# Kernel optimization log

Hardware: AMD Instinct MI355X
Metric: run time of the kernel (lower is better)

## Reference

```python
import jax, jax.numpy as jnp
import numpy as np

LN_EPS = 1e-5

def _ln(x):
    # haiku LayerNorm([-1], create_scale=False, create_offset=False)
    mu = x.mean(axis=-1, keepdims=True)
    var = x.var(axis=-1, keepdims=True)
    return (x - mu) * jax.lax.rsqrt(var + LN_EPS)

def setup_inputs() -> dict:
    key = jax.random.key(0)
    ks = jax.random.split(key, 10)
    N, L, P = 512, 256, 64
    inp = {
        "local": jax.random.normal(ks[0], (N, L), jnp.float32),
        "pair": jax.random.normal(ks[1], (N, N, P), jnp.float32),
        "mask": jax.random.randint(ks[2], (N,), 0, 2, jnp.int32),
        "W_pair_gate": jax.random.normal(ks[3], (P, 2 * P), jnp.float32) / np.sqrt(P),
        "W_pair_value": jax.random.normal(ks[4], (P, 2 * P), jnp.float32) / np.sqrt(P),
        "W_left_gate": jax.random.normal(ks[5], (L, 2 * P), jnp.float32) / np.sqrt(L),
        "W_left_value": jax.random.normal(ks[6], (L, 2 * P), jnp.float32) / np.sqrt(L),
        "W_right_gate": jax.random.normal(ks[7], (L, 2 * P), jnp.float32) / np.sqrt(L),
        "W_right_value": jax.random.normal(ks[8], (L, 2 * P), jnp.float32) / np.sqrt(L),
        "W_out": jax.random.normal(ks[9], (3 * P, P), jnp.float32) / np.sqrt(3 * P),
    }
    return inp

def reference(local, pair, mask, W_pair_gate, W_pair_value, W_left_gate,
              W_left_value, W_right_gate, W_right_value, W_out):
    maskb = mask.astype(bool)
    pair_mask = maskb[:, None] & maskb[None, :]                  # (N, N)
    l = _ln(local)                                               # (N, L)
    p = _ln(pair)                                                # (N, N, P)
    pair_gate = p @ W_pair_gate                                  # (N, N, 2P)
    pair_value = p @ W_pair_value                                # (N, N, 2P)
    # left: broadcast local over axis 0/1, gelu-gate, mask, reduce over j
    left_gate = jax.nn.gelu((l @ W_left_gate)[:, None] + pair_gate)
    left_value = (l @ W_left_value)[None, :] + pair_value
    left = jnp.where(pair_mask[..., None], left_gate * left_value, 0).sum(axis=1)  # (N, 2P)
    right_gate = jax.nn.gelu((l @ W_right_gate)[None, :] + pair_gate)
    right_value = (l @ W_right_value)[:, None] + pair_value
    right = jnp.where(pair_mask[..., None], right_gate * right_value, 0).sum(axis=0)  # (N, 2P)
    paired_pseudo_local = _ln(left[:, None] + right[None, :])    # (N, N, 2P)
    pair_hidden = jnp.concatenate((p, paired_pseudo_local), axis=-1)  # (N, N, 3P)
    return pair_hidden @ W_out                                   # (N, N, P)
```

## Files before the change

### kernel.cpp

```cpp
#include <hip/hip_runtime.h>
#include <math.h>

#define LN_EPS 1e-5f


typedef __bf16 bf16x8 __attribute__((ext_vector_type(8)));
typedef float f32x16 __attribute__((ext_vector_type(16)));

__device__ __forceinline__ float gelu_f(float x) {
    float x2 = x * x;
    float e = __builtin_amdgcn_exp2f(x * fmaf(0.10294423f, x2, 2.3022079f));
    float r = __builtin_amdgcn_rcpf(e + 1.0f);
    return fmaf(-x, r, x);
}

__global__ __launch_bounds__(256) void kA(
    const float* __restrict__ loc,
    const float* __restrict__ Wlg, const float* __restrict__ Wlv,
    const float* __restrict__ Wrg, const float* __restrict__ Wrv,
    float* __restrict__ proj, const int* __restrict__ mask,
    int* __restrict__ act, float* __restrict__ left, float* __restrict__ right) {
    const int t = threadIdx.x;
    if (blockIdx.x == 64) {
        if (blockIdx.y == 1) {
            float4 z = {0.f, 0.f, 0.f, 0.f};
            for (int idx = t; idx < 16384; idx += 256) ((float4*)left)[idx] = z;
        } else if (blockIdx.y == 2) {
            float4 z = {0.f, 0.f, 0.f, 0.f};
            for (int idx = t; idx < 16384; idx += 256) ((float4*)right)[idx] = z;
        } else if (blockIdx.y == 0) {
            __shared__ int cnt_sh[8];
            const int lane = t & 63, wv = t >> 6;
            int msave[2];
            unsigned long long bsave[2];
#pragma unroll
            for (int ch = 0; ch < 2; ++ch) {
                int m = (mask[ch * 256 + t] != 0);
                unsigned long long b = __ballot(m);
                if (lane == 0) cnt_sh[ch * 4 + wv] = __popcll(b);
                msave[ch] = m;
                bsave[ch] = b;
            }
            __syncthreads();
#pragma unroll
            for (int ch = 0; ch < 2; ++ch) {
                int base = 0;
                for (int u = 0; u < ch * 4 + wv; ++u) base += cnt_sh[u];
                int pos = base + __popcll(bsave[ch] & ((1ull << lane) - 1ull));
                if (msave[ch]) act[1 + pos] = ch * 256 + t;
            }
            if (t == 0) {
                int ctot = 0;
                for (int u = 0; u < 8; ++u) ctot += cnt_sh[u];
                act[0] = ctot;
            }
        }
        return;
    }
    __shared__ float ln_sh[8][260];
    __shared__ float red_sh[128][9];
    const int i0 = blockIdx.x * 8;
    const int mat = blockIdx.y;
    const float* __restrict__ W = (mat == 0) ? Wlg : (mat == 1) ? Wlv
                                 : (mat == 2) ? Wrg : Wrv;
    {
        int row = t >> 5, l32 = t & 31;
        const float4* src = (const float4*)(loc + (i0 + row) * 256);
        float4 v0 = src[l32 * 2];
        float4 v1 = src[l32 * 2 + 1];
        float s = (v0.x + v0.y) + (v0.z + v0.w) + (v1.x + v1.y) + (v1.z + v1.w);
        float ss = v0.x * v0.x + v0.y * v0.y + v0.z * v0.z + v0.w * v0.w +
                   v1.x * v1.x + v1.y * v1.y + v1.z * v1.z + v1.w * v1.w;
#pragma unroll
        for (int off = 1; off < 32; off <<= 1) {
            s += __shfl_xor(s, off);
            ss += __shfl_xor(ss, off);
        }
        float mu = s * (1.f / 256.f);
        float rs = rsqrtf(ss * (1.f / 256.f) - mu * mu + LN_EPS);
        float4 o0, o1;
        o0.x = (v0.x - mu) * rs; o0.y = (v0.y - mu) * rs;
        o0.z = (v0.z - mu) * rs; o0.w = (v0.w - mu) * rs;
        o1.x = (v1.x - mu) * rs; o1.y = (v1.y - mu) * rs;
        o1.z = (v1.z - mu) * rs; o1.w = (v1.w - mu) * rs;
        *(float4*)&ln_sh[row][l32 * 8] = o0;
        *(float4*)&ln_sh[row][l32 * 8 + 4] = o1;
    }
    __syncthreads();

    const int n = t & 127;
    const int kh = t >> 7;
    float acc[8] = {0.f, 0.f, 0.f, 0.f, 0.f, 0.f, 0.f, 0.f};
#pragma unroll 2
    for (int c = 0; c < 32; ++c) {
        const int kc = kh * 128 + c * 4;
        float w0 = W[(kc + 0) * 128 + n];
        float w1 = W[(kc + 1) * 128 + n];
        float w2 = W[(kc + 2) * 128 + n];
        float w3 = W[(kc + 3) * 128 + n];
#pragma unroll
        for (int r = 0; r < 8; ++r) {
            float4 l4 = *(const float4*)&ln_sh[r][kc];
            acc[r] += l4.x * w0 + l4.y * w1 + l4.z * w2 + l4.w * w3;
        }
    }
    if (kh == 1) {
#pragma unroll
        for (int r = 0; r < 8; ++r) red_sh[n][r] = acc[r];
    }
    __syncthreads();
    if (kh == 0) {
#pragma unroll
        for (int r = 0; r < 8; ++r)
            proj[mat * 65536 + (i0 + r) * 128 + n] = acc[r] + red_sh[n][r];
    }
}

#define KB_TI 4
__global__ __launch_bounds__(256) void kB(
    const float* __restrict__ pair, const int* __restrict__ act,
    const float* __restrict__ Wg, const float* __restrict__ Wv,
    const float* __restrict__ lg, const float* __restrict__ lv,
    const float* __restrict__ rg, const float* __restrict__ rv,
    float* __restrict__ left, float* __restrict__ right) {
    __shared__ __bf16 A_sh[2][32][72];
    __shared__ int ji_sh[32];
    __shared__ int ii_sh[KB_TI];

    const int cnt = act[0];
    const int j0 = blockIdx.x * 32;
    const int ibase = blockIdx.y * KB_TI;
    if (j0 >= cnt || ibase >= cnt) return;
    const int nact = min(KB_TI, cnt - ibase);

    const int t = threadIdx.x;
    const int lane = t & 63;
    const int w = t >> 6;
    const int c = lane & 31;
    const int half = lane >> 5;
    const int n = w * 32 + c;

    if (t < 32) ji_sh[t] = act[1 + min(j0 + t, cnt - 1)];
    if (t >= 64 && t < 64 + KB_TI) ii_sh[t - 64] = act[1 + min(ibase + (t - 64), cnt - 1)];
    __syncthreads();

    bf16x8 bg[4], bv[4];
#pragma unroll
    for (int kt = 0; kt < 4; ++kt) {
        bf16x8 vg, vv;
#pragma unroll
        for (int e = 0; e < 8; ++e) {
            int kr = kt * 16 + half * 8 + e;
            vg[e] = (__bf16)Wg[kr * 128 + n];
            vv[e] = (__bf16)Wv[kr * 128 + n];
        }
        bg[kt] = vg; bv[kt] = vv;
    }

    float lvr[16], rgr[16];
    unsigned jmask = 0;
#pragma unroll
    for (int r = 0; r < 16; ++r) {
        int m = 4 * half + (r & 3) + 8 * (r >> 2);
        int j = ji_sh[m];
        lvr[r] = lv[j * 128 + n];
        rgr[r] = rg[j * 128 + n];
        if (j0 + m < cnt) jmask |= (1u << r);
    }

    const int srow = t >> 3;
    const int kseg = (t & 7) * 8;
    float4 p0, p1;
    float plg, prv;
    {
        int iF = ii_sh[0];
        const float* src = pair + ((size_t)iF * 512 + ji_sh[srow]) * 64 + kseg;
        p0 = *(const float4*)src;
        p1 = *(const float4*)(src + 4);
        plg = lg[iF * 128 + n];
        prv = rv[iF * 128 + n];
    }

    auto lnwrite = [&](int buf) {
        float s = (p0.x + p0.y) + (p0.z + p0.w) + (p1.x + p1.y) + (p1.z + p1.w);
        float ss = p0.x * p0.x + p0.y * p0.y + p0.z * p0.z + p0.w * p0.w +
                   p1.x * p1.x + p1.y * p1.y + p1.z * p1.z + p1.w * p1.w;
        s += __shfl_xor(s, 1); ss += __shfl_xor(ss, 1);
        s += __shfl_xor(s, 2); ss += __shfl_xor(ss, 2);
        s += __shfl_xor(s, 4); ss += __shfl_xor(ss, 4);
        float mu = s * (1.f / 64.f);
        float rs = rsqrtf(ss * (1.f / 64.f) - mu * mu + LN_EPS);
        bf16x8 o;
        o[0] = (__bf16)((p0.x - mu) * rs); o[1] = (__bf16)((p0.y - mu) * rs);
        o[2] = (__bf16)((p0.z - mu) * rs); o[3] = (__bf16)((p0.w - mu) * rs);
        o[4] = (__bf16)((p1.x - mu) * rs); o[5] = (__bf16)((p1.y - mu) * rs);
        o[6] = (__bf16)((p1.z - mu) * rs); o[7] = (__bf16)((p1.w - mu) * rs);
        *(bf16x8*)&A_sh[buf][srow][kseg] = o;
    };
    lnwrite(0);
    __syncthreads();

    float racc[16];
#pragma unroll
    for (int r = 0; r < 16; ++r) racc[r] = 0.f;

    for (int ii = 0; ii < nact; ++ii) {
        const int i = ii_sh[ii];
        const float lgi = plg;
        const float rvi = prv;
        if (ii + 1 < nact) {
            int iF = ii_sh[ii + 1];
            const float* src = pair + ((size_t)iF * 512 + ji_sh[srow]) * 64 + kseg;
            p0 = *(const float4*)src;
            p1 = *(const float4*)(src + 4);
            plg = lg[iF * 128 + n];
            prv = rv[iF * 128 + n];
        }

        f32x16 ag = {}; f32x16 av = {};
#pragma unroll
        for (int kt = 0; kt < 4; ++kt) {
            bf16x8 af = *(const bf16x8*)&A_sh[ii & 1][c][kt * 16 + half * 8];
            ag = __builtin_amdgcn_mfma_f32_32x32x16_bf16(af, bg[kt], ag, 0, 0, 0);
            av = __builtin_amdgcn_mfma_f32_32x32x16_bf16(af, bv[kt], av, 0, 0, 0);
        }

        float lsum = 0.f;
#pragma unroll
        for (int r = 0; r < 16; ++r) {
            float pg = ag[r], pv = av[r];
            float lres = gelu_f(lgi + pg) * (lvr[r] + pv);
            float rres = gelu_f(rgr[r] + pg) * (rvi + pv);
            lsum += ((jmask >> r) & 1) ? lres : 0.f;
            racc[r] += rres;
        }
        float tot = lsum + __shfl_xor(lsum, 32);
        if (lane < 32) atomicAdd(&left[i * 128 + n], tot);

        if (ii + 1 < nact) lnwrite((ii + 1) & 1);
        __syncthreads();
    }

#pragma unroll
    for (int r = 0; r < 16; ++r) {
        if ((jmask >> r) & 1) {
            int m = 4 * half + (r & 3) + 8 * (r >> 2);
            atomicAdd(&right[ji_sh[m] * 128 + n], racc[r]);
        }
    }
}

__global__ __launch_bounds__(256) void kD(
    const float* __restrict__ left, const float* __restrict__ right,
    const float* __restrict__ W_out,
    float* __restrict__ Aw, float* __restrict__ Bw,
    float* __restrict__ rsArr, float* __restrict__ rmArr,
    float* __restrict__ cs) {
    const int bx = blockIdx.x;
    const int t = threadIdx.x;
    if (bx < 256) {
        __shared__ float l_sh[32][68];
        __shared__ float r_sh[32][68];
        const int tx = t & 15, ty = t >> 4;
        const int i0 = (bx & 15) * 32, j0 = (bx >> 4) * 32;
        float acc00 = 0.f, acc01 = 0.f, acc10 = 0.f, acc11 = 0.f;
        float sL0 = 0.f, ssL0 = 0.f, sL1 = 0.f, ssL1 = 0.f;
        float sR0 = 0.f, ssR0 = 0.f, sR1 = 0.f, ssR1 = 0.f;
        for (int kc = 0; kc < 128; kc += 64) {
            __syncthreads();
#pragma unroll
            for (int u = 0; u < 2; ++u) {
                int fi = t + u * 256;
                int row = fi >> 4, kq = (fi & 15) * 4;
                float4 lv4 = *(const float4*)(left + (i0 + row) * 128 + kc + kq);
                float4 rv4 = *(const float4*)(right + (j0 + row) * 128 + kc + kq);
                *(float4*)&l_sh[row][kq] = lv4;
                *(float4*)&r_sh[row][kq] = rv4;
            }
            __syncthreads();
#pragma unroll 8
            for (int k = 0; k < 64; ++k) {
                float l0 = l_sh[ty * 2 + 0][k], l1 = l_sh[ty * 2 + 1][k];
                float r0 = r_sh[tx * 2 + 0][k], r1 = r_sh[tx * 2 + 1][k];
                acc00 += l0 * r0; acc01 += l0 * r1;
                acc10 += l1 * r0; acc11 += l1 * r1;
                sL0 += l0; ssL0 += l0 * l0;
                sL1 += l1; ssL1 += l1 * l1;
                sR0 += r0; ssR0 += r0 * r0;
                sR1 += r1; ssR1 += r1 * r1;
            }
        }
        {
            float sLa[2] = {sL0, sL1}, ssLa[2] = {ssL0, ssL1};
            float sRb[2] = {sR0, sR1}, ssRb[2] = {ssR0, ssR1};
            float accv[2][2] = {{acc00, acc01}, {acc10, acc11}};
#pragma unroll
            for (int a = 0; a < 2; ++a) {
#pragma unroll
                for (int b = 0; b < 2; ++b) {
                    float mu = (sLa[a] + sRb[b]) * (1.f / 128.f);
                    float var = fmaf(-mu, mu,
                                     (ssLa[a] + 2.f * accv[a][b] + ssRb[b]) * (1.f / 128.f));
                    float rs = rsqrtf(var + LN_EPS);
                    size_t idx = (size_t)(i0 + ty * 2 + a) * 512 + (j0 + tx * 2 + b);
                    rsArr[idx] = rs;
                    rmArr[idx] = rs * mu;
                }
            }
        }
    } else {
        const int id = bx - 256;
        const int which = id >> 8;
        const int sub = t >> 7;
        const int tt = t & 127;
        const int r = (id & 255) * 2 + sub;
        const float* src = which ? right : left;
        __shared__ float row_sh[2][128];
        row_sh[sub][tt] = src[r * 128 + tt];
        __syncthreads();
        if (tt < 64) {
            float a = 0.f;
            const float* W2 = W_out + 64 * 64;
#pragma unroll 8
            for (int m = 0; m < 128; ++m) a += row_sh[sub][m] * W2[m * 64 + tt];
            (which ? Bw : Aw)[r * 64 + tt] = a;
        }
        if (id == 0 && t < 64) {
            float c0 = 0.f, c1 = 0.f;
            for (int k = 0; k < 64; ++k) c0 += W_out[k * 64 + t];
            for (int m = 0; m < 128; ++m) c1 += W_out[(64 + m) * 64 + t];
            cs[t] = c0;
            cs[64 + t] = c1;
        }
    }
}

__global__ __launch_bounds__(256) void kC(
    const float* __restrict__ pair, const float* __restrict__ Wout,
    const float* __restrict__ Aw, const float* __restrict__ Bw,
    const float* __restrict__ rsArr, const float* __restrict__ rmArr,
    const float* __restrict__ cs, float* __restrict__ out) {
    const int t = threadIdx.x;
    const int lane = t & 63;
    const int w = t >> 6;
    const int c = lane & 31;
    const int half = lane >> 5;
    const int i0 = blockIdx.x * 4;
    const int j0 = blockIdx.y * 64;
    const int mt = w & 1;
    const int nt = w >> 1;
    const int n = nt * 32 + c;
    const int jrow = j0 + mt * 32 + c;

    const float* __restrict__ abase = pair + ((size_t)i0 * 512 + jrow) * 64 + half * 8;

    float4 va[8], vb[8];
#pragma unroll
    for (int kt = 0; kt < 4; ++kt) {
        va[2 * kt] = *(const float4*)(abase + kt * 16);
        va[2 * kt + 1] = *(const float4*)(abase + kt * 16 + 4);
    }

    bf16x8 bo[4];
#pragma unroll
    for (int kt = 0; kt < 4; ++kt) {
        bf16x8 bb;
#pragma unroll
        for (int e = 0; e < 8; ++e)
            bb[e] = (__bf16)Wout[(kt * 16 + half * 8 + e) * 64 + n];
        bo[kt] = bb;
    }
    float Bv[16];
#pragma unroll
    for (int r = 0; r < 16; ++r) {
        int jp = j0 + mt * 32 + 4 * half + (r & 3) + 8 * (r >> 2);
        Bv[r] = Bw[jp * 64 + n];
    }
    const float cs1n = cs[64 + n];

    auto body = [&](float4 (&cur)[8], float4 (&nxt)[8], int ii) {
        if (ii < 3) {
            const float* src = abase + (size_t)(ii + 1) * 512 * 64;
#pragma unroll
            for (int kt = 0; kt < 4; ++kt) {
                nxt[2 * kt] = *(const float4*)(src + kt * 16);
                nxt[2 * kt + 1] = *(const float4*)(src + kt * 16 + 4);
            }
        }
        const int i = i0 + ii;
        const float A_in = Aw[i * 64 + n];

        float s = 0.f, ss = 0.f;
#pragma unroll
        for (int u = 0; u < 8; ++u) {
            s += (cur[u].x + cur[u].y) + (cur[u].z + cur[u].w);
            ss += cur[u].x * cur[u].x + cur[u].y * cur[u].y +
                  cur[u].z * cur[u].z + cur[u].w * cur[u].w;
        }
        s += __shfl_xor(s, 32);
        ss += __shfl_xor(ss, 32);
        float mu = s * (1.f / 64.f);
        float rs = rsqrtf(ss * (1.f / 64.f) - mu * mu + LN_EPS);

        f32x16 acc = {};
#pragma unroll
        for (int kt = 0; kt < 4; ++kt) {
            bf16x8 af;
#pragma unroll
            for (int u = 0; u < 2; ++u) {
                float4 vv = cur[2 * kt + u];
                af[u * 4 + 0] = (__bf16)((vv.x - mu) * rs);
                af[u * 4 + 1] = (__bf16)((vv.y - mu) * rs);
                af[u * 4 + 2] = (__bf16)((vv.z - mu) * rs);
                af[u * 4 + 3] = (__bf16)((vv.w - mu) * rs);
            }
            acc = __builtin_amdgcn_mfma_f32_32x32x16_bf16(af, bo[kt], acc, 0, 0, 0);
        }

#pragma unroll
        for (int r = 0; r < 16; ++r) {
            int jp = j0 + mt * 32 + 4 * half + (r & 3) + 8 * (r >> 2);
            size_t idx = (size_t)i * 512 + jp;
            float rsv = rsArr[idx];
            float rmv = rmArr[idx];
            out[idx * 64 + n] =
                fmaf(rsv, A_in + Bv[r], fmaf(-rmv, cs1n, acc[r]));
        }
    };
    body(va, vb, 0);
    body(vb, va, 1);
    body(va, vb, 2);
    body(vb, va, 3);
}

extern "C" void kernel_launch(void* const* d_in, const int* in_sizes, int n_in,
                              void* d_out, int out_size, void* d_ws, size_t ws_size,
                              hipStream_t stream) {
    const float* loc  = (const float*)d_in[0];
    const float* pair = (const float*)d_in[1];
    const int*   mask = (const int*)d_in[2];
    const float* Wpg  = (const float*)d_in[3];
    const float* Wpv  = (const float*)d_in[4];
    const float* Wlg  = (const float*)d_in[5];
    const float* Wlv  = (const float*)d_in[6];
    const float* Wrg  = (const float*)d_in[7];
    const float* Wrv  = (const float*)d_in[8];
    const float* Wout = (const float*)d_in[9];
    float* out = (float*)d_out;
    float* ws = (float*)d_ws;

    float* proj  = ws;
    float* left  = ws + 262144;
    float* right = ws + 327680;
    float* Aw    = ws + 393216;
    float* Bw    = ws + 425984;
    float* rsA   = ws + 458752;
    float* rmA   = ws;
    float* cs    = ws + 722944;
    int*   act   = (int*)(ws + 723072);

    kA<<<dim3(65, 4), 256, 0, stream>>>(loc, Wlg, Wlv, Wrg, Wrv, proj,
                                        mask, act, left, right);
    kB<<<dim3(16, 128), 256, 0, stream>>>(pair, act, Wpg, Wpv,
                                          proj, proj + 65536, proj + 131072,
                                          proj + 196608, left, right);
    kD<<<768, 256, 0, stream>>>(left, right, Wout, Aw, Bw, rsA, rmA, cs);
    kC<<<dim3(128, 8), 256, 0, stream>>>(pair, Wout, Aw, Bw, rsA, rmA, cs, out);
}
```

Before: 190.9 us.

## Privatize right-side atomic accumulation into eight partial buffers reduced in kD

The right-reduction atomics in kB now go to one of eight private copies of the right buffer, chosen by blockIdx.y, instead of a single shared buffer. kD sums the eight partials when it loads right. The aim is to cut atomic contention on the same addresses. It also vectorizes kD's shared-memory inner loop with float4 reads and packs rs/rm into one interleaved float2 array read by kC. The cost is more zeroing work in kA, an extra 8x read of the right partials in kD, and a larger workspace.

After: 200.9 us. 5.2% more time.

```diff
diff --git a/kernel.cpp b/kernel.cpp
--- a/kernel.cpp
+++ b/kernel.cpp
@@ -19,7 +19,7 @@
     const float* __restrict__ Wlg, const float* __restrict__ Wlv,
     const float* __restrict__ Wrg, const float* __restrict__ Wrv,
     float* __restrict__ proj, const int* __restrict__ mask,
-    int* __restrict__ act, float* __restrict__ left, float* __restrict__ right) {
+    int* __restrict__ act, float* __restrict__ left, float* __restrict__ rightP) {
     const int t = threadIdx.x;
     if (blockIdx.x == 64) {
         if (blockIdx.y == 1) {
@@ -27,7 +27,10 @@
             for (int idx = t; idx < 16384; idx += 256) ((float4*)left)[idx] = z;
         } else if (blockIdx.y == 2) {
             float4 z = {0.f, 0.f, 0.f, 0.f};
-            for (int idx = t; idx < 16384; idx += 256) ((float4*)right)[idx] = z;
+            for (int idx = t; idx < 65536; idx += 256) ((float4*)rightP)[idx] = z;
+        } else if (blockIdx.y == 3) {
+            float4 z = {0.f, 0.f, 0.f, 0.f};
+            for (int idx = 65536 + t; idx < 131072; idx += 256) ((float4*)rightP)[idx] = z;
         } else if (blockIdx.y == 0) {
             __shared__ int cnt_sh[8];
             const int lane = t & 63, wv = t >> 6;
@@ -122,7 +125,7 @@
     const float* __restrict__ Wg, const float* __restrict__ Wv,
     const float* __restrict__ lg, const float* __restrict__ lv,
     const float* __restrict__ rg, const float* __restrict__ rv,
-    float* __restrict__ left, float* __restrict__ right) {
+    float* __restrict__ left, float* __restrict__ rightP) {
     __shared__ __bf16 A_sh[2][32][72];
     __shared__ int ji_sh[32];
     __shared__ int ii_sh[KB_TI];
@@ -241,21 +244,21 @@
         __syncthreads();
     }
 
+    float* rp = rightP + (blockIdx.y & 7) * 65536;
 #pragma unroll
     for (int r = 0; r < 16; ++r) {
         if ((jmask >> r) & 1) {
             int m = 4 * half + (r & 3) + 8 * (r >> 2);
-            atomicAdd(&right[ji_sh[m] * 128 + n], racc[r]);
+            atomicAdd(&rp[ji_sh[m] * 128 + n], racc[r]);
         }
     }
 }
 
 __global__ __launch_bounds__(256) void kD(
-    const float* __restrict__ left, const float* __restrict__ right,
+    const float* __restrict__ left, const float* __restrict__ rightP,
     const float* __restrict__ W_out,
     float* __restrict__ Aw, float* __restrict__ Bw,
-    float* __restrict__ rsArr, float* __restrict__ rmArr,
-    float* __restrict__ cs) {
+    float* __restrict__ rsrm, float* __restrict__ cs) {
     const int bx = blockIdx.x;
     const int t = threadIdx.x;
     if (bx < 256) {
@@ -273,21 +276,35 @@
                 int fi = t + u * 256;
                 int row = fi >> 4, kq = (fi & 15) * 4;
                 float4 lv4 = *(const float4*)(left + (i0 + row) * 128 + kc + kq);
-                float4 rv4 = *(const float4*)(right + (j0 + row) * 128 + kc + kq);
+                float4 rv4 = {0.f, 0.f, 0.f, 0.f};
+#pragma unroll
+                for (int g = 0; g < 8; ++g) {
+                    float4 pv = *(const float4*)(rightP + g * 65536 +
+                                                 (j0 + row) * 128 + kc + kq);
+                    rv4.x += pv.x; rv4.y += pv.y; rv4.z += pv.z; rv4.w += pv.w;
+                }
                 *(float4*)&l_sh[row][kq] = lv4;
                 *(float4*)&r_sh[row][kq] = rv4;
             }
             __syncthreads();
-#pragma unroll 8
-            for (int k = 0; k < 64; ++k) {
-                float l0 = l_sh[ty * 2 + 0][k], l1 = l_sh[ty * 2 + 1][k];
-                float r0 = r_sh[tx * 2 + 0][k], r1 = r_sh[tx * 2 + 1][k];
-                acc00 += l0 * r0; acc01 += l0 * r1;
-                acc10 += l1 * r0; acc11 += l1 * r1;
-                sL0 += l0; ssL0 += l0 * l0;
-                sL1 += l1; ssL1 += l1 * l1;
-                sR0 += r0; ssR0 += r0 * r0;
-                sR1 += r1; ssR1 += r1 * r1;
+#pragma unroll
+            for (int k4 = 0; k4 < 64; k4 += 4) {
+                float4 l0 = *(const float4*)&l_sh[ty * 2 + 0][k4];
+                float4 l1 = *(const float4*)&l_sh[ty * 2 + 1][k4];
+                float4 r0 = *(const float4*)&r_sh[tx * 2 + 0][k4];
+                float4 r1 = *(const float4*)&r_sh[tx * 2 + 1][k4];
+                acc00 += l0.x * r0.x + l0.y * r0.y + l0.z * r0.z + l0.w * r0.w;
+                acc01 += l0.x * r1.x + l0.y * r1.y + l0.z * r1.z + l0.w * r1.w;
+                acc10 += l1.x * r0.x + l1.y * r0.y + l1.z * r0.z + l1.w * r0.w;
+                acc11 += l1.x * r1.x + l1.y * r1.y + l1.z * r1.z + l1.w * r1.w;
+                sL0 += (l0.x + l0.y) + (l0.z + l0.w);
+                ssL0 += l0.x * l0.x + l0.y * l0.y + l0.z * l0.z + l0.w * l0.w;
+                sL1 += (l1.x + l1.y) + (l1.z + l1.w);
+                ssL1 += l1.x * l1.x + l1.y * l1.y + l1.z * l1.z + l1.w * l1.w;
+                sR0 += (r0.x + r0.y) + (r0.z + r0.w);
+                ssR0 += r0.x * r0.x + r0.y * r0.y + r0.z * r0.z + r0.w * r0.w;
+                sR1 += (r1.x + r1.y) + (r1.z + r1.w);
+                ssR1 += r1.x * r1.x + r1.y * r1.y + r1.z * r1.z + r1.w * r1.w;
             }
         }
         {
@@ -303,8 +320,8 @@
                                      (ssLa[a] + 2.f * accv[a][b] + ssRb[b]) * (1.f / 128.f));
                     float rs = rsqrtf(var + LN_EPS);
                     size_t idx = (size_t)(i0 + ty * 2 + a) * 512 + (j0 + tx * 2 + b);
-                    rsArr[idx] = rs;
-                    rmArr[idx] = rs * mu;
+                    float2 v; v.x = rs; v.y = rs * mu;
+                    ((float2*)rsrm)[idx] = v;
                 }
             }
         }
@@ -314,9 +331,16 @@
         const int sub = t >> 7;
         const int tt = t & 127;
         const int r = (id & 255) * 2 + sub;
-        const float* src = which ? right : left;
         __shared__ float row_sh[2][128];
-        row_sh[sub][tt] = src[r * 128 + tt];
+        float v;
+        if (which) {
+            v = 0.f;
+#pragma unroll
+            for (int g = 0; g < 8; ++g) v += rightP[g * 65536 + r * 128 + tt];
+        } else {
+            v = left[r * 128 + tt];
+        }
+        row_sh[sub][tt] = v;
         __syncthreads();
         if (tt < 64) {
             float a = 0.f;
@@ -338,7 +362,7 @@
 __global__ __launch_bounds__(256) void kC(
     const float* __restrict__ pair, const float* __restrict__ Wout,
     const float* __restrict__ Aw, const float* __restrict__ Bw,
-    const float* __restrict__ rsArr, const float* __restrict__ rmArr,
+    const float* __restrict__ rsrm,
     const float* __restrict__ cs, float* __restrict__ out) {
     const int t = threadIdx.x;
     const int lane = t & 63;
@@ -421,10 +445,9 @@
         for (int r = 0; r < 16; ++r) {
             int jp = j0 + mt * 32 + 4 * half + (r & 3) + 8 * (r >> 2);
             size_t idx = (size_t)i * 512 + jp;
-            float rsv = rsArr[idx];
-            float rmv = rmArr[idx];
+            float2 rr = ((const float2*)rsrm)[idx];
             out[idx * 64 + n] =
-                fmaf(rsv, A_in + Bv[r], fmaf(-rmv, cs1n, acc[r]));
+                fmaf(rr.x, A_in + Bv[r], fmaf(-rr.y, cs1n, acc[r]));
         }
     };
     body(va, vb, 0);
@@ -449,21 +472,20 @@
     float* out = (float*)d_out;
     float* ws = (float*)d_ws;
 
-    float* proj  = ws;
-    float* left  = ws + 262144;
-    float* right = ws + 327680;
-    float* Aw    = ws + 393216;
-    float* Bw    = ws + 425984;
-    float* rsA   = ws + 458752;
-    float* rmA   = ws;
-    float* cs    = ws + 722944;
-    int*   act   = (int*)(ws + 723072);
+    float* proj   = ws;
+    float* left   = ws + 262144;
+    float* Aw     = ws + 393216;
+    float* Bw     = ws + 425984;
+    float* rsrm   = ws + 458752;
+    float* cs     = ws + 983040;
+    int*   act    = (int*)(ws + 983168);
+    float* rightP = ws + 1048576;
 
     kA<<<dim3(65, 4), 256, 0, stream>>>(loc, Wlg, Wlv, Wrg, Wrv, proj,
-                                        mask, act, left, right);
+                                        mask, act, left, rightP);
     kB<<<dim3(16, 128), 256, 0, stream>>>(pair, act, Wpg, Wpv,
                                           proj, proj + 65536, proj + 131072,
-                                          proj + 196608, left, right);
-    kD<<<768, 256, 0, stream>>>(left, right, Wout, Aw, Bw, rsA, rmA, cs);
-    kC<<<dim3(128, 8), 256, 0, stream>>>(pair, Wout, Aw, Bw, rsA, rmA, cs, out);
-}
+                                          proj + 196608, left, rightP);
+    kD<<<768, 256, 0, stream>>>(left, rightP, Wout, Aw, Bw, rsrm, cs);
+    kC<<<dim3(128, 8), 256, 0, stream>>>(pair, Wout, Aw, Bw, rsrm, cs, out);
+}
```
